# Kernel optimization log

Hardware: AMD Instinct MI355X
Metric: run time of the kernel (lower is better)

The kernel has to match this reference:

```python
import jax, jax.numpy as jnp
import numpy as np

B, T, N, KH, DH, KS = 8, 64, 128, 8, 64, 3  # batch, num_step, num_vertex, heads, head_dim, kernel
D = KH * DH
EPS = 1e-5


def setup_inputs() -> dict:
    key = jax.random.key(0)
    ks = jax.random.split(key, 8)
    s = 0.02
    return {
        "X": jax.random.normal(ks[0], (B, T, N, D), dtype=jnp.float32),
        # causal conv Q/K: torch Conv2d weight [out, in, 1, ks]
        "Wq": jax.random.normal(ks[1], (D, D, 1, KS), dtype=jnp.float32) * s,
        "bq": jnp.zeros((D,), jnp.float32),
        "gq": jnp.ones((D,), jnp.float32),
        "betaq": jnp.zeros((D,), jnp.float32),
        "mq": jnp.zeros((D,), jnp.float32),
        "vq": jnp.ones((D,), jnp.float32),
        "Wk": jax.random.normal(ks[2], (D, D, 1, KS), dtype=jnp.float32) * s,
        "bk": jnp.zeros((D,), jnp.float32),
        "gk": jnp.ones((D,), jnp.float32),
        "betak": jnp.zeros((D,), jnp.float32),
        "mk": jnp.zeros((D,), jnp.float32),
        "vk": jnp.ones((D,), jnp.float32),
        # torch Linear weights [out, in]
        "Wv": jax.random.normal(ks[3], (D, D), dtype=jnp.float32) * s,
        "bv": jnp.zeros((D,), jnp.float32),
        "Wo": jax.random.normal(ks[4], (D, D), dtype=jnp.float32) * s,
        "bo": jnp.zeros((D,), jnp.float32),
    }


def _causal_conv(x, W, b):
    # x: [B, D, N, T]; left-pad time by ks-1 == torch pad-both-then-slice[:-pad]
    pad = W.shape[-1] - 1
    y = jax.lax.conv_general_dilated(
        x, W, window_strides=(1, 1), padding=((0, 0), (pad, 0)),
        dimension_numbers=("NCHW", "OIHW", "NCHW"))
    return y + b[None, :, None, None]


def _bn(x, g, beta, m, v):
    # eval-mode BatchNorm2d over channel dim 1
    inv = jax.lax.rsqrt(v + EPS)
    return (x - m[None, :, None, None]) * (g * inv)[None, :, None, None] + beta[None, :, None, None]


def reference(X, Wq, bq, gq, betaq, mq, vq, Wk, bk, gk, betak, mk, vk, Wv, bv, Wo, bo):
    b, t, n, dm = X.shape
    X_ = X.transpose(0, 3, 2, 1)                       # [B, D, N, T]
    q = _bn(_causal_conv(X_, Wq, bq), gq, betaq, mq, vq).transpose(0, 3, 2, 1)  # [B,T,N,D]
    k = _bn(_causal_conv(X_, Wk, bk), gk, betak, mk, vk).transpose(0, 3, 2, 1)  # [B,T,N,D]
    v = jnp.einsum("btnd,ed->btne", X, Wv) + bv        # FC_v
    # split heads (equivalent to split/cat along batch in the original)
    qh = q.reshape(b, t, n, KH, DH)
    kh = k.reshape(b, t, n, KH, DH)
    vh = v.reshape(b, t, n, KH, DH)
    scores = jnp.einsum("bqnhd,bpnhd->bnhqp", qh, kh) * (DH ** -0.5)  # [B,N,H,T,T]
    attn = jax.nn.softmax(scores, axis=-1)
    out = jnp.einsum("bnhqp,bpnhd->bqnhd", attn, vh).reshape(b, t, n, dm)
    out = jnp.einsum("btnd,ed->btne", out, Wo) + bo    # FC
    return out  # [B, T, N, D]
```

## Files before the change

### kernel.cpp

```cpp
#include <hip/hip_runtime.h>

typedef unsigned short u16;
typedef u16    u16x4  __attribute__((ext_vector_type(4)));
typedef u16    u16x8  __attribute__((ext_vector_type(8)));
typedef __bf16 bf16x8 __attribute__((ext_vector_type(8)));
typedef float  f32x4  __attribute__((ext_vector_type(4)));

#define DEV static __device__ __forceinline__

DEV float bf2f(u16 h) {
    union { unsigned int u; float f; } c; c.u = ((unsigned int)h) << 16; return c.f;
}
DEV u16 f2bf(float f) {
    union { float f; unsigned int u; } c; c.f = f;
    unsigned int u = c.u + 0x7FFFu + ((c.u >> 16) & 1u);
    return (u16)(u >> 16);
}
DEV bf16x8 ld8(const u16* p) {
    return __builtin_bit_cast(bf16x8, *(const u16x8*)p);
}
DEV void gload_lds16(const u16* g, u16* l) {
    __builtin_amdgcn_global_load_lds((__attribute__((address_space(1))) void*)g,
                                     (__attribute__((address_space(3))) void*)l,
                                     16, 0, 0);
}
DEV void bar() {
    asm volatile("" ::: "memory");
    __builtin_amdgcn_s_barrier();
    asm volatile("" ::: "memory");
}
#define VMCNT(n) asm volatile("s_waitcnt vmcnt(" #n ")" ::: "memory")

__global__ __launch_bounds__(256) void f32_to_bf16(
    const float* __restrict__ src, u16* __restrict__ dst, int n)
{
    int i = (blockIdx.x * 256 + threadIdx.x) * 4;
    if (i < n) {
        f32x4 v = *(const f32x4*)(src + i);
        u16x4 o;
        o[0] = f2bf(v[0]); o[1] = f2bf(v[1]); o[2] = f2bf(v[2]); o[3] = f2bf(v[3]);
        *(u16x4*)(dst + i) = o;
    }
}

__global__ __launch_bounds__(256) void prep_weights(
    const float* __restrict__ Wq, const float* __restrict__ gq, const float* __restrict__ vq,
    const float* __restrict__ Wk, const float* __restrict__ gk, const float* __restrict__ vk,
    u16* __restrict__ Wqt, u16* __restrict__ Wkt)
{
    int idx = blockIdx.x * 256 + threadIdx.x;
    int mat = idx >= 786432;
    int rem = idx - mat * 786432;
    int tap = rem / 262144;
    int oi  = rem - tap * 262144;
    int o = oi >> 9, i = oi & 511;
    const float* W = mat ? Wk : Wq;
    const float* g = mat ? gk : gq;
    const float* v = mat ? vk : vq;
    float s = g[o] * rsqrtf(v[o] + 1e-5f) * (mat ? 1.0f : 0.125f);
    float w = W[(o * 512 + i) * 3 + tap] * s;
    (mat ? Wkt : Wqt)[(o * 3 + tap) * 512 + i] = f2bf(w);
}

__global__ __launch_bounds__(256) void prep_bias(
    const float* bq, const float* gq, const float* betaq, const float* mq, const float* vq,
    const float* bk, const float* gk, const float* betak, const float* mk, const float* vk,
    float* __restrict__ biasq, float* __restrict__ biask, u16* __restrict__ zb)
{
    int o = blockIdx.x * 256 + threadIdx.x;
    if (o < 512) {
        float sq = gq[o] * rsqrtf(vq[o] + 1e-5f);
        biasq[o] = ((bq[o] - mq[o]) * sq + betaq[o]) * 0.125f;
        float sk = gk[o] * rsqrtf(vk[o] + 1e-5f);
        biask[o] = (bk[o] - mk[o]) * sk + betak[o];
    }
    if (blockIdx.x == 0 && threadIdx.x < 64) zb[threadIdx.x] = 0;
}

__global__ __launch_bounds__(512, 1) void qkv8(
    const u16* __restrict__ Xb,
    const u16* __restrict__ Wq3, const u16* __restrict__ Wk3, const u16* __restrict__ Wv1,
    const float* __restrict__ biasq, const float* __restrict__ biask, const float* __restrict__ bv,
    const u16* __restrict__ zbuf,
    u16* __restrict__ Qa, u16* __restrict__ Ka, u16* __restrict__ Va, int b0)
{
    __shared__ __align__(16) u16 As[2 * 16384];
    __shared__ __align__(16) u16 Bs[2 * 16384];

    const int total = gridDim.x;
    const int cpx   = total >> 3;
    const int s     = blockIdx.x;
    const int w     = (s & 7) * cpx + (s >> 3);
    const int wc    = w % 6;
    const int bt    = w / 6;
    const int which = wc >> 1;
    const int cb    = (wc & 1) * 256;
    const int tpair = bt & 31;
    const int brel  = bt >> 5;
    const int b     = b0 + brel;

    const int tid  = threadIdx.x;
    const int wave = tid >> 6;
    const int lane = tid & 63;
    const int l15  = lane & 15;
    const int q4   = lane >> 4;
    const int wn   = wave;

    const u16* WB = (which == 0) ? Wq3 : (which == 1) ? Wk3 : Wv1;
    const int  KW = (which == 2) ? 512 : 1536;
    const int  NT = (which == 2) ? 8 : 24;

    f32x4 acc[16][2];
#pragma unroll
    for (int a = 0; a < 16; ++a)
#pragma unroll
        for (int ni = 0; ni < 2; ++ni) acc[a][ni] = f32x4{0.f, 0.f, 0.f, 0.f};

    auto stageA = [&](int kt, int bufp, int h) {
        int tap  = (which == 2) ? 0 : (kt >> 3);
        int kb   = (which == 2) ? (kt << 6) : ((kt & 7) << 6);
        int tsrc = 2 * tpair + h + ((which == 2) ? 0 : (tap - 2));
#pragma unroll
        for (int j = 0; j < 2; ++j) {
            int slot = h * 1024 + j * 512 + tid;
            int r = slot >> 3, sl = slot & 7;
            const u16* src = (tsrc < 0) ? zbuf
                : Xb + ((size_t)((b * 64 + tsrc) * 128 + (r & 127))) * 512 + kb
                     + ((sl ^ (r & 7)) << 3);
            gload_lds16(src, As + bufp * 16384 + slot * 8);
        }
    };
    auto stageB = [&](int kt, int bufp, int h) {
#pragma unroll
        for (int j = 0; j < 2; ++j) {
            int slot = h * 1024 + j * 512 + tid;
            int r = slot >> 3, sl = slot & 7;
            const u16* src = WB + (size_t)(cb + r) * KW + (kt << 6)
                           + ((sl ^ (r & 7)) << 3);
            gload_lds16(src, Bs + bufp * 16384 + slot * 8);
        }
    };

#define PHASE_READ_B() \
    _Pragma("unroll") \
    for (int ni = 0; ni < 2; ++ni) { \
        _Pragma("unroll") \
        for (int ks = 0; ks < 2; ++ks) { \
            int rr = wn * 32 + ni * 16 + l15; \
            bfr[ni][ks] = ld8(Bcur + ((rr * 64 + ks * 32 + q4 * 8) ^ ((l15 & 7) << 3))); \
        } \
    }

#define PHASE_READ_A(q) \
    _Pragma("unroll") \
    for (int mi = 0; mi < 4; ++mi) { \
        _Pragma("unroll") \
        for (int ks = 0; ks < 2; ++ks) { \
            int rr = (q) * 64 + mi * 16 + l15; \
            af[mi][ks] = ld8(Acur + ((rr * 64 + ks * 32 + q4 * 8) ^ ((l15 & 7) << 3))); \
        } \
    }

#define PHASE_MFMA(q) \
    __builtin_amdgcn_s_setprio(1); \
    _Pragma("unroll") \
    for (int ks = 0; ks < 2; ++ks) \
        _Pragma("unroll") \
        for (int mi = 0; mi < 4; ++mi) \
            _Pragma("unroll") \
            for (int ni = 0; ni < 2; ++ni) \
                acc[(q) * 4 + mi][ni] = __builtin_amdgcn_mfma_f32_16x16x32_bf16( \
                    af[mi][ks], bfr[ni][ks], acc[(q) * 4 + mi][ni], 0, 0, 0); \
    __builtin_amdgcn_s_setprio(0);

    stageB(0, 0, 0); stageB(0, 0, 1);
    stageA(0, 0, 0); stageA(0, 0, 1);
    VMCNT(2);
    bar();

    for (int kt = 0; kt < NT; ++kt) {
        const int cur = kt & 1, nxt = cur ^ 1;
        const bool pf = (kt + 1 < NT);
        const u16* Acur = As + cur * 16384;
        const u16* Bcur = Bs + cur * 16384;
        bf16x8 af[4][2], bfr[2][2];

        PHASE_READ_B();
        PHASE_READ_A(0);
        if (pf) stageB(kt + 1, nxt, 0);
        bar();
        PHASE_MFMA(0);
        bar();

        PHASE_READ_A(1);
        if (pf) stageB(kt + 1, nxt, 1);
        bar();
        PHASE_MFMA(1);
        VMCNT(4);
        bar();

        PHASE_READ_A(2);
        if (pf) stageA(kt + 1, nxt, 0);
        bar();
        PHASE_MFMA(2);
        bar();

        PHASE_READ_A(3);
        if (pf) stageA(kt + 1, nxt, 1);
        bar();
        PHASE_MFMA(3);
        VMCNT(2);
        bar();
    }

#undef PHASE_READ_B
#undef PHASE_READ_A
#undef PHASE_MFMA

    const float* biasp = (which == 0) ? biasq : (which == 1) ? biask : bv;
    float bias2[2];
#pragma unroll
    for (int ni = 0; ni < 2; ++ni) bias2[ni] = biasp[cb + wn * 32 + ni * 16 + l15];
    u16* Outp = (which == 0) ? Qa : (which == 1) ? Ka : Va;
#pragma unroll
    for (int a = 0; a < 16; ++a) {
#pragma unroll
        for (int ni = 0; ni < 2; ++ni) {
            int c = cb + wn * 32 + ni * 16 + l15;
            int h = c >> 6, dd = c & 63;
#pragma unroll
            for (int r = 0; r < 4; ++r) {
                int row = a * 16 + q4 * 4 + r;
                int n = row & 127, tt = 2 * tpair + (row >> 7);
                float val = acc[a][ni][r] + bias2[ni];
                Outp[((((size_t)(brel * 128 + n)) * 8 + h) * 64 + tt) * 64 + dd] = f2bf(val);
            }
        }
    }
}

__global__ __launch_bounds__(256) void attn_kernel(
    const u16* __restrict__ Qa, const u16* __restrict__ Ka, const u16* __restrict__ Va,
    u16* __restrict__ AO)
{
    __shared__ __align__(16) u16 Qs[64 * 72];
    __shared__ __align__(16) u16 Ks[64 * 72];
    __shared__ __align__(16) u16 Vt[64 * 72];
    __shared__ __align__(16) u16 Ps[64 * 72];

    const int h = blockIdx.x, n = blockIdx.y, brel = blockIdx.z;
    const int tid = threadIdx.x, wave = tid >> 6, lane = tid & 63;
    const int l15 = lane & 15, q4 = lane >> 4;
    const size_t base = ((size_t)((brel * 128 + n) * 8 + h)) * 4096;

#pragma unroll
    for (int i = 0; i < 2; i++) {
        int chunk = i * 256 + tid;
        int row = chunk >> 3, kc = chunk & 7;
        u16x8 vq = *(const u16x8*)(Qa + base + chunk * 8);
        u16x8 vk = *(const u16x8*)(Ka + base + chunk * 8);
        u16x8 vv = *(const u16x8*)(Va + base + chunk * 8);
        *(u16x8*)(Qs + row * 72 + kc * 8) = vq;
        *(u16x8*)(Ks + row * 72 + kc * 8) = vk;
#pragma unroll
        for (int j = 0; j < 8; j++) Vt[(kc * 8 + j) * 72 + row] = vv[j];
    }
    __syncthreads();

    f32x4 s[4];
#pragma unroll
    for (int ni = 0; ni < 4; ni++) s[ni] = f32x4{0.f, 0.f, 0.f, 0.f};
    bf16x8 aq[2];
#pragma unroll
    for (int ks = 0; ks < 2; ks++)
        aq[ks] = ld8(Qs + (wave * 16 + l15) * 72 + ks * 32 + q4 * 8);
#pragma unroll
    for (int ni = 0; ni < 4; ni++) {
        int p = ni * 16 + l15;
#pragma unroll
        for (int ks = 0; ks < 2; ks++) {
            bf16x8 bk8 = ld8(Ks + p * 72 + ks * 32 + q4 * 8);
            s[ni] = __builtin_amdgcn_mfma_f32_16x16x32_bf16(aq[ks], bk8, s[ni], 0, 0, 0);
        }
    }

    float rmax[4], rsum[4], inv[4];
#pragma unroll
    for (int r = 0; r < 4; r++)
        rmax[r] = fmaxf(fmaxf(s[0][r], s[1][r]), fmaxf(s[2][r], s[3][r]));
#pragma unroll
    for (int m = 1; m < 16; m <<= 1)
#pragma unroll
        for (int r = 0; r < 4; r++)
            rmax[r] = fmaxf(rmax[r], __shfl_xor(rmax[r], m, 64));
    float e[4][4];
#pragma unroll
    for (int r = 0; r < 4; r++) rsum[r] = 0.f;
#pragma unroll
    for (int ni = 0; ni < 4; ni++)
#pragma unroll
        for (int r = 0; r < 4; r++) {
            e[ni][r] = __expf(s[ni][r] - rmax[r]);
            rsum[r] += e[ni][r];
        }
#pragma unroll
    for (int m = 1; m < 16; m <<= 1)
#pragma unroll
        for (int r = 0; r < 4; r++)
            rsum[r] += __shfl_xor(rsum[r], m, 64);
#pragma unroll
    for (int r = 0; r < 4; r++) inv[r] = 1.0f / rsum[r];

#pragma unroll
    for (int ni = 0; ni < 4; ni++)
#pragma unroll
        for (int r = 0; r < 4; r++)
            Ps[(wave * 16 + q4 * 4 + r) * 72 + ni * 16 + l15] = f2bf(e[ni][r]);
    __syncthreads();

    f32x4 o[4];
#pragma unroll
    for (int ni = 0; ni < 4; ni++) o[ni] = f32x4{0.f, 0.f, 0.f, 0.f};
    bf16x8 ap[2];
#pragma unroll
    for (int ks = 0; ks < 2; ks++)
        ap[ks] = ld8(Ps + (wave * 16 + l15) * 72 + ks * 32 + q4 * 8);
#pragma unroll
    for (int ni = 0; ni < 4; ni++) {
        int dd = ni * 16 + l15;
#pragma unroll
        for (int ks = 0; ks < 2; ks++) {
            bf16x8 bv8 = ld8(Vt + dd * 72 + ks * 32 + q4 * 8);
            o[ni] = __builtin_amdgcn_mfma_f32_16x16x32_bf16(ap[ks], bv8, o[ni], 0, 0, 0);
        }
    }

#pragma unroll
    for (int ni = 0; ni < 4; ni++) {
        int dd = ni * 16 + l15;
#pragma unroll
        for (int r = 0; r < 4; r++) {
            int tt = wave * 16 + q4 * 4 + r;
            AO[base + tt * 64 + dd] = f2bf(o[ni][r] * inv[r]);
        }
    }
}

__global__ __launch_bounds__(256) void proj_gemm(
    const u16* __restrict__ AO, const u16* __restrict__ Wo, const float* __restrict__ bo,
    float* __restrict__ Out, int b0)
{
    __shared__ __align__(16) u16 As[128 * 64];
    __shared__ __align__(16) u16 Bs[128 * 64];

    const int cb   = blockIdx.x * 128;
    const int rt   = blockIdx.y;
    const int brel = rt >> 6;
    const int b    = b0 + brel;
    const int t    = rt & 63;

    const int tid  = threadIdx.x;
    const int wave = tid >> 6;
    const int lane = tid & 63;
    const int wm   = (wave & 1) * 64;
    const int wn   = (wave >> 1) * 64;
    const int l31  = lane & 31;
    const int q5   = lane >> 5;

    typedef float f32x16_t __attribute__((ext_vector_type(16)));
    f32x16_t acc[2][2];
#pragma unroll
    for (int mi = 0; mi < 2; mi++)
#pragma unroll
        for (int ni = 0; ni < 2; ni++)
#pragma unroll
            for (int e = 0; e < 16; e++) acc[mi][ni][e] = 0.f;

    for (int kk = 0; kk < 512; kk += 64) {
        __syncthreads();
#pragma unroll
        for (int i = 0; i < 4; ++i) {
            int p   = i * 256 + tid;
            int row = p >> 3;
            int sl  = (p & 7) ^ (row & 7);
            int k   = kk + sl * 8;
            int hh  = k >> 6, d0 = k & 63;
            const u16* ga = AO + ((((size_t)(brel * 128 + row)) * 8 + hh) * 64 + t) * 64 + d0;
            gload_lds16(ga, As + p * 8);
            gload_lds16(Wo + (size_t)(cb + row) * 512 + k, Bs + p * 8);
        }
        __syncthreads();

#pragma unroll
        for (int half = 0; half < 2; ++half) {
            bf16x8 af[2][2], bf[2][2];
#pragma unroll
            for (int mi = 0; mi < 2; mi++) {
                int r = wm + mi * 32 + l31;
#pragma unroll
                for (int j = 0; j < 2; j++) {
                    int k2 = half * 2 + j;
                    af[mi][j] = ld8(As + ((r * 64 + k2 * 16 + q5 * 8) ^ ((r & 7) << 3)));
                }
            }
#pragma unroll
            for (int ni = 0; ni < 2; ni++) {
                int c = wn + ni * 32 + l31;
#pragma unroll
                for (int j = 0; j < 2; j++) {
                    int k2 = half * 2 + j;
                    bf[ni][j] = ld8(Bs + ((c * 64 + k2 * 16 + q5 * 8) ^ ((c & 7) << 3)));
                }
            }
#pragma unroll
            for (int j = 0; j < 2; j++)
#pragma unroll
                for (int mi = 0; mi < 2; mi++)
#pragma unroll
                    for (int ni = 0; ni < 2; ni++)
                        acc[mi][ni] = __builtin_amdgcn_mfma_f32_32x32x16_bf16(
                            af[mi][j], bf[ni][j], acc[mi][ni], 0, 0, 0);
        }
    }

#pragma unroll
    for (int mi = 0; mi < 2; mi++) {
#pragma unroll
        for (int ni = 0; ni < 2; ni++) {
            int c = cb + wn + ni * 32 + l31;
            float bias = bo[c];
#pragma unroll
            for (int r = 0; r < 16; r++) {
                int n = wm + mi * 32 + (r & 3) + ((r >> 2) << 3) + (q5 << 2);
                float val = acc[mi][ni][r] + bias;
                size_t idx = (((size_t)(b * 64 + t)) * 128 + n) * 512 + c;
                Out[idx] = val;
            }
        }
    }
}

extern "C" void kernel_launch(void* const* d_in, const int* in_sizes, int n_in,
                              void* d_out, int out_size, void* d_ws, size_t ws_size,
                              hipStream_t stream)
{
    const float* X     = (const float*)d_in[0];
    const float* Wq    = (const float*)d_in[1];
    const float* bq    = (const float*)d_in[2];
    const float* gq    = (const float*)d_in[3];
    const float* betaq = (const float*)d_in[4];
    const float* mq    = (const float*)d_in[5];
    const float* vq    = (const float*)d_in[6];
    const float* Wk    = (const float*)d_in[7];
    const float* bk    = (const float*)d_in[8];
    const float* gk    = (const float*)d_in[9];
    const float* betak = (const float*)d_in[10];
    const float* mk    = (const float*)d_in[11];
    const float* vk    = (const float*)d_in[12];
    const float* Wv    = (const float*)d_in[13];
    const float* bv    = (const float*)d_in[14];
    const float* Wo    = (const float*)d_in[15];
    const float* bo    = (const float*)d_in[16];
    float* outp = (float*)d_out;
    u16*   ws   = (u16*)d_ws;

    const size_t XTOT   = 33554432;
    const size_t XSLICE = 4194304;

    const bool big = ws_size >= (size_t)206000000;

    u16 *Xb, *Qa, *Ka, *Wqt;
    if (big) {
        Xb  = ws;
        Qa  = ws + XTOT;
        Ka  = Qa + XTOT;
        Wqt = Ka + XTOT;
    } else {
        Xb  = ws;
        Qa  = ws + XSLICE;
        Ka  = Qa + XSLICE;
        Wqt = Ka + XSLICE;
    }
    u16* Wkt = Wqt + 786432;
    u16* Wvb = Wkt + 786432;
    u16* Wob = Wvb + 262144;
    float* biasq = (float*)(Wob + 262144);
    float* biask = biasq + 512;
    u16*   zbuf  = (u16*)(biask + 512);

    hipLaunchKernelGGL(prep_weights, dim3(6144), dim3(256), 0, stream,
                       Wq, gq, vq, Wk, gk, vk, Wqt, Wkt);
    hipLaunchKernelGGL(prep_bias, dim3(2), dim3(256), 0, stream,
                       bq, gq, betaq, mq, vq, bk, gk, betak, mk, vk, biasq, biask, zbuf);
    hipLaunchKernelGGL(f32_to_bf16, dim3(256), dim3(256), 0, stream, Wv, Wvb, 262144);
    hipLaunchKernelGGL(f32_to_bf16, dim3(256), dim3(256), 0, stream, Wo, Wob, 262144);

    if (big) {
        u16* Va = (u16*)d_out;
        hipLaunchKernelGGL(f32_to_bf16, dim3(32768), dim3(256), 0, stream,
                           X, Xb, (int)XTOT);
        hipLaunchKernelGGL(qkv8, dim3(1536), dim3(512), 0, stream,
                           Xb, Wqt, Wkt, Wvb, biasq, biask, bv, zbuf, Qa, Ka, Va, 0);
        hipLaunchKernelGGL(attn_kernel, dim3(8, 128, 8), dim3(256), 0, stream,
                           Qa, Ka, Va, Qa);
        hipLaunchKernelGGL(proj_gemm, dim3(4, 512), dim3(256), 0, stream,
                           Qa, Wob, bo, outp, 0);
    } else {
        for (int p = 0; p < 8; ++p) {
            u16* Va = (u16*)d_out + (size_t)p * 2 * XSLICE;
            hipLaunchKernelGGL(f32_to_bf16, dim3(4096), dim3(256), 0, stream,
                               X + (size_t)p * XSLICE, Xb, (int)XSLICE);
            hipLaunchKernelGGL(qkv8, dim3(192), dim3(512), 0, stream,
                               Xb - (size_t)p * XSLICE, Wqt, Wkt, Wvb,
                               biasq, biask, bv, zbuf, Qa, Ka, Va, p);
            hipLaunchKernelGGL(attn_kernel, dim3(8, 128, 1), dim3(256), 0, stream,
                               Qa, Ka, Va, Qa);
            hipLaunchKernelGGL(proj_gemm, dim3(4, 64), dim3(256), 0, stream,
                               Qa, Wob, bo, outp, p);
        }
    }
}
```

Before: 614.3 us.

## Retile projection GEMM to 2x4 wave grid with k-split LDS halves

Changes the wave layout of the QKV projection GEMM from 8 waves each owning a 32-column strip across all 256 rows to a 2x4 grid where each wave owns a 128x64 tile. The LDS staging is also reorganised into two 32-wide k-halves with a new XOR swizzle, and the prefetch and wait schedule is reworked around those halves. The intent is to cut LDS fragment reads per MFMA by sharing A and B fragments more evenly. The trade-off is more B fragments held in registers, plus more complex vmcnt accounting that could mis-synchronise.

```diff
diff --git a/kernel.cpp b/kernel.cpp
--- a/kernel.cpp
+++ b/kernel.cpp
@@ -104,78 +104,71 @@
     const int lane = tid & 63;
     const int l15  = lane & 15;
     const int q4   = lane >> 4;
-    const int wn   = wave;
+    const int wm   = (wave >> 2) * 128;
+    const int wn3  = (wave & 3) * 64;
 
     const u16* WB = (which == 0) ? Wq3 : (which == 1) ? Wk3 : Wv1;
     const int  KW = (which == 2) ? 512 : 1536;
     const int  NT = (which == 2) ? 8 : 24;
 
-    f32x4 acc[16][2];
-#pragma unroll
-    for (int a = 0; a < 16; ++a)
-#pragma unroll
-        for (int ni = 0; ni < 2; ++ni) acc[a][ni] = f32x4{0.f, 0.f, 0.f, 0.f};
-
-    auto stageA = [&](int kt, int bufp, int h) {
-        int tap  = (which == 2) ? 0 : (kt >> 3);
-        int kb   = (which == 2) ? (kt << 6) : ((kt & 7) << 6);
-        int tsrc = 2 * tpair + h + ((which == 2) ? 0 : (tap - 2));
+    f32x4 acc[8][4];
+#pragma unroll
+    for (int a = 0; a < 8; ++a)
+#pragma unroll
+        for (int ni = 0; ni < 4; ++ni) acc[a][ni] = f32x4{0.f, 0.f, 0.f, 0.f};
+
+    auto stageA = [&](int kt, int bufp, int ks) {
+        int tap = (which == 2) ? 0 : (kt >> 3);
+        int kb  = ((which == 2) ? (kt << 6) : ((kt & 7) << 6)) + ks * 32;
 #pragma unroll
         for (int j = 0; j < 2; ++j) {
-            int slot = h * 1024 + j * 512 + tid;
-            int r = slot >> 3, sl = slot & 7;
+            int c = j * 512 + tid;
+            int r = c >> 2;
+            int ss = (c & 3) ^ ((r >> 1) & 3);
+            int tsrc = 2 * tpair + j + ((which == 2) ? 0 : (tap - 2));
             const u16* src = (tsrc < 0) ? zbuf
-                : Xb + ((size_t)((b * 64 + tsrc) * 128 + (r & 127))) * 512 + kb
-                     + ((sl ^ (r & 7)) << 3);
-            gload_lds16(src, As + bufp * 16384 + slot * 8);
+                : Xb + ((size_t)((b * 64 + tsrc) * 128 + (r & 127))) * 512 + kb + ss * 8;
+            gload_lds16(src, As + bufp * 16384 + ks * 8192 + c * 8);
         }
     };
-    auto stageB = [&](int kt, int bufp, int h) {
+    auto stageB = [&](int kt, int bufp, int ks) {
 #pragma unroll
         for (int j = 0; j < 2; ++j) {
-            int slot = h * 1024 + j * 512 + tid;
-            int r = slot >> 3, sl = slot & 7;
-            const u16* src = WB + (size_t)(cb + r) * KW + (kt << 6)
-                           + ((sl ^ (r & 7)) << 3);
-            gload_lds16(src, Bs + bufp * 16384 + slot * 8);
+            int c = j * 512 + tid;
+            int r = c >> 2;
+            int ss = (c & 3) ^ ((r >> 1) & 3);
+            const u16* src = WB + (size_t)(cb + r) * KW + (kt << 6) + ks * 32 + ss * 8;
+            gload_lds16(src, Bs + bufp * 16384 + ks * 8192 + c * 8);
         }
     };
 
-#define PHASE_READ_B() \
+#define READ_B(ks) \
     _Pragma("unroll") \
-    for (int ni = 0; ni < 2; ++ni) { \
-        _Pragma("unroll") \
-        for (int ks = 0; ks < 2; ++ks) { \
-            int rr = wn * 32 + ni * 16 + l15; \
-            bfr[ni][ks] = ld8(Bcur + ((rr * 64 + ks * 32 + q4 * 8) ^ ((l15 & 7) << 3))); \
-        } \
-    }
-
-#define PHASE_READ_A(q) \
+    for (int ni = 0; ni < 4; ++ni) { \
+        int rr = wn3 + ni * 16 + l15; \
+        bfr[ni] = ld8(Bcur + (ks) * 8192 + rr * 32 + ((q4 ^ ((rr >> 1) & 3)) << 3)); \
+    }
+
+#define READ_A(ks, mh) \
     _Pragma("unroll") \
-    for (int mi = 0; mi < 4; ++mi) { \
-        _Pragma("unroll") \
-        for (int ks = 0; ks < 2; ++ks) { \
-            int rr = (q) * 64 + mi * 16 + l15; \
-            af[mi][ks] = ld8(Acur + ((rr * 64 + ks * 32 + q4 * 8) ^ ((l15 & 7) << 3))); \
-        } \
-    }
-
-#define PHASE_MFMA(q) \
+    for (int f = 0; f < 4; ++f) { \
+        int rr = wm + (mh) * 64 + f * 16 + l15; \
+        af[f] = ld8(Acur + (ks) * 8192 + rr * 32 + ((q4 ^ ((rr >> 1) & 3)) << 3)); \
+    }
+
+#define PHASE_MFMA(mh) \
     __builtin_amdgcn_s_setprio(1); \
     _Pragma("unroll") \
-    for (int ks = 0; ks < 2; ++ks) \
+    for (int f = 0; f < 4; ++f) \
         _Pragma("unroll") \
-        for (int mi = 0; mi < 4; ++mi) \
-            _Pragma("unroll") \
-            for (int ni = 0; ni < 2; ++ni) \
-                acc[(q) * 4 + mi][ni] = __builtin_amdgcn_mfma_f32_16x16x32_bf16( \
-                    af[mi][ks], bfr[ni][ks], acc[(q) * 4 + mi][ni], 0, 0, 0); \
+        for (int ni = 0; ni < 4; ++ni) \
+            acc[(mh) * 4 + f][ni] = __builtin_amdgcn_mfma_f32_16x16x32_bf16( \
+                af[f], bfr[ni], acc[(mh) * 4 + f][ni], 0, 0, 0); \
     __builtin_amdgcn_s_setprio(0);
 
-    stageB(0, 0, 0); stageB(0, 0, 1);
-    stageA(0, 0, 0); stageA(0, 0, 1);
-    VMCNT(2);
+    stageA(0, 0, 0); stageB(0, 0, 0);
+    stageA(0, 0, 1); stageB(0, 0, 1);
+    VMCNT(4);
     bar();
 
     for (int kt = 0; kt < NT; ++kt) {
@@ -183,56 +176,57 @@
         const bool pf = (kt + 1 < NT);
         const u16* Acur = As + cur * 16384;
         const u16* Bcur = Bs + cur * 16384;
-        bf16x8 af[4][2], bfr[2][2];
-
-        PHASE_READ_B();
-        PHASE_READ_A(0);
+        bf16x8 af[4], bfr[4];
+
+        READ_B(0);
+        READ_A(0, 0);
+        if (pf) stageA(kt + 1, nxt, 0);
+        bar();
+        PHASE_MFMA(0);
+        bar();
+
+        READ_A(0, 1);
         if (pf) stageB(kt + 1, nxt, 0);
         bar();
+        PHASE_MFMA(1);
+        if (pf) { VMCNT(4); } else { VMCNT(0); }
+        bar();
+
+        READ_B(1);
+        READ_A(1, 0);
+        if (pf) stageA(kt + 1, nxt, 1);
+        bar();
         PHASE_MFMA(0);
         bar();
 
-        PHASE_READ_A(1);
+        READ_A(1, 1);
         if (pf) stageB(kt + 1, nxt, 1);
         bar();
         PHASE_MFMA(1);
-        VMCNT(4);
-        bar();
-
-        PHASE_READ_A(2);
-        if (pf) stageA(kt + 1, nxt, 0);
-        bar();
-        PHASE_MFMA(2);
-        bar();
-
-        PHASE_READ_A(3);
-        if (pf) stageA(kt + 1, nxt, 1);
-        bar();
-        PHASE_MFMA(3);
-        VMCNT(2);
-        bar();
-    }
-
-#undef PHASE_READ_B
-#undef PHASE_READ_A
+        if (pf) { VMCNT(4); }
+        bar();
+    }
+
+#undef READ_B
+#undef READ_A
 #undef PHASE_MFMA
 
     const float* biasp = (which == 0) ? biasq : (which == 1) ? biask : bv;
-    float bias2[2];
-#pragma unroll
-    for (int ni = 0; ni < 2; ++ni) bias2[ni] = biasp[cb + wn * 32 + ni * 16 + l15];
+    float bias4[4];
+#pragma unroll
+    for (int ni = 0; ni < 4; ++ni) bias4[ni] = biasp[cb + wn3 + ni * 16 + l15];
     u16* Outp = (which == 0) ? Qa : (which == 1) ? Ka : Va;
 #pragma unroll
-    for (int a = 0; a < 16; ++a) {
-#pragma unroll
-        for (int ni = 0; ni < 2; ++ni) {
-            int c = cb + wn * 32 + ni * 16 + l15;
+    for (int a = 0; a < 8; ++a) {
+#pragma unroll
+        for (int ni = 0; ni < 4; ++ni) {
+            int c = cb + wn3 + ni * 16 + l15;
             int h = c >> 6, dd = c & 63;
 #pragma unroll
             for (int r = 0; r < 4; ++r) {
-                int row = a * 16 + q4 * 4 + r;
+                int row = wm + (a >> 2) * 64 + (a & 3) * 16 + q4 * 4 + r;
                 int n = row & 127, tt = 2 * tpair + (row >> 7);
-                float val = acc[a][ni][r] + bias2[ni];
+                float val = acc[a][ni][r] + bias4[ni];
                 Outp[((((size_t)(brel * 128 + n)) * 8 + h) * 64 + tt) * 64 + dd] = f2bf(val);
             }
         }
```

Measured after the change: 653.3 us. 1.06x slower.
